# Kernel optimization log

Measured on AMD Instinct MI355X. Metric: run time of the kernel, lower is better.

## Reference

```python
import jax, jax.numpy as jnp
import numpy as np

# ---- model dims (match init_kwargs) ----
N_PER = 10000          # nodes per omic view
NUM_OMICS = 3
N = N_PER * NUM_OMICS  # 30000 total nodes (omic blocks are contiguous)
E = 500000             # edges
R = 6                  # num_relations
HEADS = 1
PROJ = 128             # proj_dim
H0 = 128               # hidden_channels[0]
H1 = 128               # hidden_channels[1]
LABELS = 5
IN_SIZES = [2000, 1500, 1000]
SLOPE = 0.2            # RGATConv leaky_relu negative_slope


def setup_inputs() -> dict:
    key = jax.random.key(0)
    ks = iter(jax.random.split(key, 64))

    def nrm(shape, fan_in):
        return jax.random.normal(next(ks), shape, dtype=jnp.float32) / np.float32(np.sqrt(fan_in))

    inp = {}
    for i, s in enumerate(IN_SIZES):
        inp[f"x{i}"] = jax.random.normal(next(ks), (N_PER, s), dtype=jnp.float32)
    for i, s in enumerate(IN_SIZES):
        inp[f"projW{i}"] = nrm((s, PROJ), s)
        inp[f"projb{i}"] = jnp.zeros((PROJ,), jnp.float32)
    for i in range(NUM_OMICS):
        inp[f"slW{i}"] = nrm((PROJ, H0), PROJ)
        inp[f"slb{i}"] = jnp.zeros((H0,), jnp.float32)
    # RGAT layer 1: weight [R, in, heads*out], q/k [heads*out, heads], bias [heads*out]
    inp["W1"] = nrm((R, PROJ, HEADS * H0), PROJ)
    inp["q1"] = nrm((HEADS * H0, HEADS), H0)
    inp["k1"] = nrm((HEADS * H0, HEADS), H0)
    inp["b1"] = jnp.zeros((HEADS * H0,), jnp.float32)
    # RGAT layer 2: heads=1
    inp["W2"] = nrm((R, HEADS * H0, H1), H0)
    inp["q2"] = nrm((H1, 1), H1)
    inp["k2"] = nrm((H1, 1), H1)
    inp["b2"] = jnp.zeros((H1,), jnp.float32)
    inp["lin1W"] = nrm((H1, H1), H1)
    inp["lin1b"] = jnp.zeros((H1,), jnp.float32)
    inp["lin2W"] = nrm((H1, LABELS), H1)
    inp["lin2b"] = jnp.zeros((LABELS,), jnp.float32)
    inp["edge_src"] = jax.random.randint(next(ks), (E,), 0, N, dtype=jnp.int32)
    inp["edge_dst"] = jax.random.randint(next(ks), (E,), 0, N, dtype=jnp.int32)
    inp["edge_type"] = jax.random.randint(next(ks), (E,), 0, R, dtype=jnp.int32)
    return inp


def _rgat(x, src, dst, etype, W, q, k, b, heads, out_ch):
    """PyG RGATConv: additive-self-attention, across-relation softmax, mod='f-scaled'."""
    # per-relation linear transform of all nodes, then gather per edge
    xw = jnp.einsum('nd,rdo->rno', x, W)          # [R, N, heads*out]
    out_i = xw[etype, dst]                        # [E, heads*out] (target)
    out_j = xw[etype, src]                        # [E, heads*out] (source)
    alpha = jax.nn.leaky_relu(out_i @ q + out_j @ k, SLOPE)   # [E, heads]
    # segment softmax over destination nodes
    m = jax.ops.segment_max(alpha, dst, num_segments=N)
    a = jnp.exp(alpha - m[dst])
    s = jax.ops.segment_sum(a, dst, num_segments=N)
    a = a / s[dst]
    # f-scaled: multiply by in-degree of destination
    deg = jax.ops.segment_sum(jnp.ones((a.shape[0],), a.dtype), dst, num_segments=N)
    a = a * deg[dst][:, None]
    msg = (a[:, :, None] * out_j.reshape(-1, heads, out_ch)).reshape(-1, heads * out_ch)
    return jax.ops.segment_sum(msg, dst, num_segments=N) + b


def reference(x0, x1, x2, projW0, projb0, projW1, projb1, projW2, projb2,
              slW0, slb0, slW1, slb1, slW2, slb2,
              W1, q1, k1, b1, W2, q2, k2, b2,
              lin1W, lin1b, lin2W, lin2b,
              edge_src, edge_dst, edge_type):
    # per-omic projections (ELU)
    xp0 = jax.nn.elu(x0 @ projW0 + projb0)
    xp1 = jax.nn.elu(x1 @ projW1 + projb1)
    xp2 = jax.nn.elu(x2 @ projW2 + projb2)
    x = jnp.concatenate([xp0, xp1, xp2], axis=0)  # [N, PROJ] homogeneous features
    # self-loop contributions (self_loops1 is applied after BOTH convs, on projected x,
    # as in the original forward). Omic node blocks are contiguous.
    sl = jnp.concatenate([xp0 @ slW0 + slb0, xp1 @ slW1 + slb1, xp2 @ slW2 + slb2], axis=0)
    h = jax.nn.elu(_rgat(x, edge_src, edge_dst, edge_type, W1, q1, k1, b1, HEADS, H0) + sl)
    h = jax.nn.elu(_rgat(h, edge_src, edge_dst, edge_type, W2, q2, k2, b2, 1, H1) + sl)
    # classify node_type == 0 nodes (first omic block); dropout p=0.2 is identity at eval
    z = jax.nn.elu(h[:N_PER] @ lin1W + lin1b)
    return z @ lin2W + lin2b
```

## Files before the change

kernel.cpp:

```cpp
#include <hip/hip_runtime.h>
#include <math.h>

#define N_TOTAL 30000
#define NPER 10000
#define NEDGE 500000
#define NREL 6
#define SLOPE 0.2f
#define WCAP 4

typedef __attribute__((ext_vector_type(4))) float f32x4;
typedef __attribute__((ext_vector_type(8))) short s16x8;
typedef __attribute__((ext_vector_type(4))) short s16x4;
typedef unsigned short u16;
typedef unsigned int u32;

__device__ __forceinline__ u16 f2bf(float v) {
  u32 x = __float_as_uint(v);
  u32 r = (x + 0x7fffu + ((x >> 16) & 1u)) >> 16;
  return (u16)r;
}
__device__ __forceinline__ float bf2f(u16 u) {
  return __uint_as_float(((u32)u) << 16);
}

template<bool BIAS, bool ELU, bool ADD, bool SPLITK>
__device__ __forceinline__ void gemm_core(
    const float* __restrict__ A, const u16* __restrict__ Bt,
    const float* __restrict__ bias, const float* __restrict__ add,
    float* __restrict__ C, int M, int K, int Kp, int kbeg, int kend)
{
  __shared__ char As[64 * 128];
  __shared__ char Aslo[64 * 128];
  __shared__ char Bs[128 * 128];
  const int tid = threadIdx.x;
  const int bm = blockIdx.x * 64;
  const int lane = tid & 63;
  const int wave = tid >> 6;
  const int wr = wave >> 1, wc = wave & 1;
  const int lane16 = lane & 15, lhalf = lane >> 4;

  const int a_row0 = tid >> 4;
  const int a_kc = (tid & 15) << 2;
  const int b_row0 = tid >> 3;
  const int b_kc = (tid & 7) << 3;

  float4 pa[4];
  s16x8 pb[4];

  auto LOAD = [&](int k0) {
    #pragma unroll
    for (int it = 0; it < 4; it++) {
      int gr = bm + a_row0 + it * 16, gk = k0 + a_kc;
      float4 v = make_float4(0.f, 0.f, 0.f, 0.f);
      if (gr < M && gk < K) v = *(const float4*)&A[(size_t)gr * K + gk];
      pa[it] = v;
    }
    #pragma unroll
    for (int it = 0; it < 4; it++) {
      int row = b_row0 + it * 32;
      pb[it] = *(const s16x8*)&Bt[(size_t)row * Kp + k0 + b_kc];
    }
  };

  f32x4 acc[2][4];
  #pragma unroll
  for (int mi = 0; mi < 2; mi++)
    #pragma unroll
    for (int ni = 0; ni < 4; ni++)
      #pragma unroll
      for (int q = 0; q < 4; q++) acc[mi][ni][q] = 0.f;

  LOAD(kbeg);

  for (int k0 = kbeg; k0 < kend; k0 += 64) {
    #pragma unroll
    for (int it = 0; it < 4; it++) {
      int row = a_row0 + it * 16;
      float vv[4] = {pa[it].x, pa[it].y, pa[it].z, pa[it].w};
      s16x4 hi, lo;
      #pragma unroll
      for (int j = 0; j < 4; j++) {
        u16 h = f2bf(vv[j]);
        hi[j] = (short)h;
        lo[j] = (short)f2bf(vv[j] - bf2f(h));
      }
      int boff = row * 128 + ((a_kc * 2) ^ ((row & 7) << 4));
      *(s16x4*)(As + boff) = hi;
      *(s16x4*)(Aslo + boff) = lo;
    }
    #pragma unroll
    for (int it = 0; it < 4; it++) {
      int row = b_row0 + it * 32;
      *(s16x8*)(Bs + row * 128 + ((b_kc * 2) ^ ((row & 7) << 4))) = pb[it];
    }
    __syncthreads();
    if (k0 + 64 < kend) LOAD(k0 + 64);
    #pragma unroll
    for (int kk = 0; kk < 2; kk++) {
      const int kbyte = kk * 64 + lhalf * 16;
      s16x8 afh[2], afl[2], bfr[4];
      #pragma unroll
      for (int mi = 0; mi < 2; mi++) {
        int row = wr * 32 + mi * 16 + lane16;
        int boff = row * 128 + (kbyte ^ ((row & 7) << 4));
        afh[mi] = *(const s16x8*)(As + boff);
        afl[mi] = *(const s16x8*)(Aslo + boff);
      }
      #pragma unroll
      for (int ni = 0; ni < 4; ni++) {
        int row = wc * 64 + ni * 16 + lane16;
        bfr[ni] = *(const s16x8*)(Bs + row * 128 + (kbyte ^ ((row & 7) << 4)));
      }
      #pragma unroll
      for (int mi = 0; mi < 2; mi++)
        #pragma unroll
        for (int ni = 0; ni < 4; ni++) {
          acc[mi][ni] = __builtin_amdgcn_mfma_f32_16x16x32_bf16(
              afl[mi], bfr[ni], acc[mi][ni], 0, 0, 0);
          acc[mi][ni] = __builtin_amdgcn_mfma_f32_16x16x32_bf16(
              afh[mi], bfr[ni], acc[mi][ni], 0, 0, 0);
        }
    }
    __syncthreads();
  }

  float bcol[4];
  #pragma unroll
  for (int ni = 0; ni < 4; ni++) {
    int col = wc * 64 + ni * 16 + lane16;
    if (BIAS) bcol[ni] = bias[col];
  }
  #pragma unroll
  for (int mi = 0; mi < 2; mi++) {
    #pragma unroll
    for (int q = 0; q < 4; q++) {
      int grow = bm + wr * 32 + mi * 16 + lhalf * 4 + q;
      if (grow < M) {
        #pragma unroll
        for (int ni = 0; ni < 4; ni++) {
          float v = acc[mi][ni][q];
          int col = wc * 64 + ni * 16 + lane16;
          if (BIAS) v += bcol[ni];
          if (ADD) v += add[(size_t)grow * 128 + col];
          if (!SPLITK && ELU) v = v > 0.f ? v : expm1f(v);
          C[(size_t)grow * 128 + col] = v;
        }
      }
    }
  }
}

struct GB {
  const float* A[3];
  const u16* Bt[3];
  const float* bias[3];
  const float* add[3];
  float* C[3];
  int K[3];
  int Kp[3];
};

template<bool BIAS, bool ELU, bool ADD>
__global__ __launch_bounds__(256, 2)
void gemm_mfma(GB gb, int M)
{
  int z = blockIdx.z;
  gemm_core<BIAS, ELU, ADD, false>(gb.A[z], gb.Bt[z], gb.bias[z], gb.add[z],
                                   gb.C[z], M, gb.K[z], gb.Kp[z], 0, gb.Kp[z]);
}

struct SK {
  const float* A[3];
  const u16* Bt[3];
  float* C[3];
  int K[3];
  int Kp[3];
};

__global__ __launch_bounds__(256, 2)
void gemm_splitk(SK sk, int M)
{
  int z = blockIdx.z;
  int cb = blockIdx.y * 512;
  if (cb >= sk.Kp[z]) return;
  int kend = (cb + 512 < sk.Kp[z]) ? cb + 512 : sk.Kp[z];
  float* C = sk.C[z] + (size_t)blockIdx.y * M * 128;
  gemm_core<false, false, false, true>(sk.A[z], sk.Bt[z], nullptr, nullptr,
                                       C, M, sk.K[z], sk.Kp[z], cb, kend);
}

struct RP { const float* bias[3]; int nch[3]; };

__global__ __launch_bounds__(256)
void reduce_proj(const float* __restrict__ part, RP rp, float* __restrict__ Xf)
{
  int z = blockIdx.z;
  int i = blockIdx.x * 256 + threadIdx.x;
  int c = i & 127;
  int nch = rp.nch[z];
  const float* base = part + (size_t)z * 4 * NPER * 128 + i;
  float s = 0.f;
  for (int ch = 0; ch < nch; ch++) s += base[(size_t)ch * NPER * 128];
  s += rp.bias[z][c];
  Xf[(size_t)z * NPER * 128 + i] = s > 0.f ? s : expm1f(s);
}

struct CW {
  const float* src[9];
  u16* dst[9];
  int K[9];
  int Kp[9];
};

__global__ __launch_bounds__(256)
void conv_w(CW cw) {
  int z = blockIdx.z;
  int K = cw.K[z], Kp = cw.Kp[z];
  int idx = blockIdx.x * 256 + threadIdx.x;
  if (idx >= 128 * Kp) return;
  int kq = idx >> 7, n = idx & 127;
  cw.dst[z][(size_t)n * Kp + kq] =
      (kq < K) ? f2bf(cw.src[z][(size_t)kq * 128 + n]) : (u16)0;
}

__global__ __launch_bounds__(128)
void wqk_kernel(const float* __restrict__ W, const float* __restrict__ q,
                const float* __restrict__ k, float* __restrict__ wq,
                float* __restrict__ wk)
{
  int r = blockIdx.x;
  int t = threadIdx.x;
  const float* Wr = W + (size_t)r * 128 * 128 + (size_t)t * 128;
  float aq = 0.f, ak = 0.f;
  for (int o = 0; o < 128; o++) {
    float w = Wr[o];
    aq = fmaf(w, q[o], aq);
    ak = fmaf(w, k[o], ak);
  }
  wq[r * 128 + t] = aq;
  wk[r * 128 + t] = ak;
}

__global__ __launch_bounds__(256)
void qdkd_kernel(const float* __restrict__ Xf, const float* __restrict__ wq,
                 const float* __restrict__ wk, float* __restrict__ QD,
                 float* __restrict__ KD)
{
  __shared__ float sq[NREL * 128], sk[NREL * 128];
  for (int i = threadIdx.x; i < NREL * 128; i += 256) { sq[i] = wq[i]; sk[i] = wk[i]; }
  __syncthreads();
  int n = blockIdx.x * 256 + threadIdx.x;
  if (n >= N_TOTAL) return;
  float aq[NREL], ak[NREL];
  #pragma unroll
  for (int r = 0; r < NREL; r++) { aq[r] = 0.f; ak[r] = 0.f; }
  for (int kc = 0; kc < 128; kc += 4) {
    float4 x = *(const float4*)&Xf[(size_t)n * 128 + kc];
    #pragma unroll
    for (int r = 0; r < NREL; r++) {
      aq[r] += x.x * sq[r * 128 + kc] + x.y * sq[r * 128 + kc + 1]
             + x.z * sq[r * 128 + kc + 2] + x.w * sq[r * 128 + kc + 3];
      ak[r] += x.x * sk[r * 128 + kc] + x.y * sk[r * 128 + kc + 1]
             + x.z * sk[r * 128 + kc + 2] + x.w * sk[r * 128 + kc + 3];
    }
  }
  #pragma unroll
  for (int r = 0; r < NREL; r++) {
    QD[(size_t)r * N_TOTAL + n] = aq[r];
    KD[(size_t)r * N_TOTAL + n] = ak[r];
  }
}

__global__ __launch_bounds__(256)
void edge_count(const int* __restrict__ dst, int* __restrict__ cnt) {
  int e = blockIdx.x * 256 + threadIdx.x;
  if (e < NEDGE) atomicAdd(&cnt[dst[e]], 1);
}

__global__ __launch_bounds__(1024)
void scan_kernel(const int* __restrict__ cnt, int* __restrict__ off,
                 int* __restrict__ cur) {
  __shared__ int ps[1024];
  const int t = threadIdx.x;
  const int CH = (N_TOTAL + 1023) / 1024;
  const int base = t * CH;
  int s = 0;
  for (int i = 0; i < CH; i++) {
    int idx = base + i;
    if (idx < N_TOTAL) s += cnt[idx];
  }
  ps[t] = s;
  __syncthreads();
  for (int o = 1; o < 1024; o <<= 1) {
    int v = (t >= o) ? ps[t - o] : 0;
    __syncthreads();
    ps[t] += v;
    __syncthreads();
  }
  int run = ps[t] - s;
  for (int i = 0; i < CH; i++) {
    int idx = base + i;
    if (idx < N_TOTAL) {
      off[idx] = run; cur[idx] = run;
      run += cnt[idx];
    }
  }
  if (t == 1023) off[N_TOTAL] = run;
}

__global__ __launch_bounds__(256)
void edge_fill(const int* __restrict__ dst, const int* __restrict__ src,
               const int* __restrict__ et, int* __restrict__ cur,
               int* __restrict__ meta) {
  int e = blockIdx.x * 256 + threadIdx.x;
  if (e >= NEDGE) return;
  int p = atomicAdd(&cur[dst[e]], 1);
  meta[p] = src[e] | (et[e] << 15);
}

__global__ __launch_bounds__(256)
void csr_aggw(const int* __restrict__ off, const int* __restrict__ meta,
              const float* __restrict__ qd, const float* __restrict__ kd,
              const float* __restrict__ xrow, float* __restrict__ agg)
{
  const int d = blockIdx.x * 4 + (threadIdx.x >> 6);
  const int lane = threadIdx.x & 63;
  if (d >= N_TOTAL) return;
  const int n0 = off[d];
  const int deg = off[d + 1] - n0;

  float2 accr[NREL];
  #pragma unroll
  for (int r = 0; r < NREL; r++) accr[r] = make_float2(0.f, 0.f);

  float qrow[NREL];
  #pragma unroll
  for (int r = 0; r < NREL; r++) qrow[r] = qd[r * N_TOTAL + d];

  if (deg > 0) {
    if (deg <= 64 * WCAP) {
      int mreg[WCAP];
      float areg[WCAP];
      const int nc = (deg + 63) >> 6;
      float lmax = -3.0e38f;
      #pragma unroll
      for (int c = 0; c < WCAP; c++) {
        mreg[c] = 0; areg[c] = -3.0e38f;
        int i = c * 64 + lane;
        if (c < nc && i < deg) {
          int mm = meta[n0 + i];
          int s_ = mm & 0x7FFF, t = mm >> 15;
          float a = qrow[t] + kd[t * N_TOTAL + s_];
          a = (a > 0.f) ? a : SLOPE * a;
          mreg[c] = mm; areg[c] = a;
          lmax = fmaxf(lmax, a);
        }
      }
      #pragma unroll
      for (int m = 32; m; m >>= 1) lmax = fmaxf(lmax, __shfl_xor(lmax, m));
      float lsum = 0.f;
      #pragma unroll
      for (int c = 0; c < WCAP; c++) {
        int i = c * 64 + lane;
        if (c < nc && i < deg) {
          areg[c] = expf(areg[c] - lmax);
          lsum += areg[c];
        }
      }
      #pragma unroll
      for (int m = 32; m; m >>= 1) lsum += __shfl_xor(lsum, m);
      const float scale = (float)deg / lsum;
      for (int i = 0; i < deg; i++) {
        int c = i >> 6, l = i & 63;
        float cf = 0.f; int mm = 0;
        #pragma unroll
        for (int cc = 0; cc < WCAP; cc++) {
          if (cc == c) { cf = __shfl(areg[cc], l); mm = __shfl(mreg[cc], l); }
        }
        cf *= scale;
        int s_ = mm & 0x7FFF, t = mm >> 15;
        float2 v = *(const float2*)&xrow[(size_t)s_ * 128 + lane * 2];
        float2 cv = make_float2(cf * v.x, cf * v.y);
        #pragma unroll
        for (int r = 0; r < NREL; r++) {
          bool hit = (t == r);
          accr[r].x += hit ? cv.x : 0.f;
          accr[r].y += hit ? cv.y : 0.f;
        }
      }
    } else {
      float m = -3.0e38f;
      for (int i = 0; i < deg; i++) {
        int mm = meta[n0 + i];
        int s_ = mm & 0x7FFF, t = mm >> 15;
        float a = qrow[t] + kd[t * N_TOTAL + s_];
        a = (a > 0.f) ? a : SLOPE * a;
        m = fmaxf(m, a);
      }
      float ssum = 0.f;
      for (int i = 0; i < deg; i++) {
        int mm = meta[n0 + i];
        int s_ = mm & 0x7FFF, t = mm >> 15;
        float a = qrow[t] + kd[t * N_TOTAL + s_];
        a = (a > 0.f) ? a : SLOPE * a;
        ssum += expf(a - m);
      }
      const float scale = (float)deg / ssum;
      for (int i = 0; i < deg; i++) {
        int mm = meta[n0 + i];
        int s_ = mm & 0x7FFF, t = mm >> 15;
        float a = qrow[t] + kd[t * N_TOTAL + s_];
        a = (a > 0.f) ? a : SLOPE * a;
        float cf = expf(a - m) * scale;
        float2 v = *(const float2*)&xrow[(size_t)s_ * 128 + lane * 2];
        float2 cv = make_float2(cf * v.x, cf * v.y);
        #pragma unroll
        for (int r = 0; r < NREL; r++) {
          bool hit = (t == r);
          accr[r].x += hit ? cv.x : 0.f;
          accr[r].y += hit ? cv.y : 0.f;
        }
      }
    }
  }
  #pragma unroll
  for (int r = 0; r < NREL; r++)
    *(float2*)&agg[((size_t)d * NREL + r) * 128 + lane * 2] = accr[r];
}

__global__ __launch_bounds__(256)
void lin2_kernel(const float* __restrict__ z, const float* __restrict__ W,
                 const float* __restrict__ b, float* __restrict__ out)
{
  int row = blockIdx.x * 4 + (threadIdx.x >> 6);
  int lane = threadIdx.x & 63;
  if (row >= NPER) return;
  float p[5] = {0.f, 0.f, 0.f, 0.f, 0.f};
  #pragma unroll
  for (int h = 0; h < 2; h++) {
    int kidx = lane + h * 64;
    float zv = z[(size_t)row * 128 + kidx];
    #pragma unroll
    for (int j = 0; j < 5; j++) p[j] = fmaf(zv, W[kidx * 5 + j], p[j]);
  }
  #pragma unroll
  for (int mm = 32; mm; mm >>= 1)
    #pragma unroll
    for (int j = 0; j < 5; j++) p[j] += __shfl_xor(p[j], mm);
  if (lane == 0) {
    #pragma unroll
    for (int j = 0; j < 5; j++) out[(size_t)row * 5 + j] = p[j] + b[j];
  }
}

extern "C" void kernel_launch(void* const* d_in, const int* in_sizes, int n_in,
                              void* d_out, int out_size, void* d_ws, size_t ws_size,
                              hipStream_t stream) {
  const float* xs[3] = {(const float*)d_in[0], (const float*)d_in[1], (const float*)d_in[2]};
  const float* projW[3] = {(const float*)d_in[3], (const float*)d_in[5], (const float*)d_in[7]};
  const float* projb[3] = {(const float*)d_in[4], (const float*)d_in[6], (const float*)d_in[8]};
  const float* slW[3]   = {(const float*)d_in[9], (const float*)d_in[11], (const float*)d_in[13]};
  const float* slb[3]   = {(const float*)d_in[10], (const float*)d_in[12], (const float*)d_in[14]};
  const float* W1 = (const float*)d_in[15];
  const float* q1 = (const float*)d_in[16];
  const float* k1 = (const float*)d_in[17];
  const float* b1 = (const float*)d_in[18];
  const float* W2 = (const float*)d_in[19];
  const float* q2 = (const float*)d_in[20];
  const float* k2 = (const float*)d_in[21];
  const float* b2 = (const float*)d_in[22];
  const float* lin1W = (const float*)d_in[23];
  const float* lin1b = (const float*)d_in[24];
  const float* lin2W = (const float*)d_in[25];
  const float* lin2b = (const float*)d_in[26];
  const int* esrc = (const int*)d_in[27];
  const int* edst = (const int*)d_in[28];
  const int* etyp = (const int*)d_in[29];

  char* wp = (char*)d_ws;
  auto alloc = [&](size_t bytes) -> char* {
    char* p = wp; wp += (bytes + 255) & ~(size_t)255; return p;
  };
  float* Xf  = (float*)alloc((size_t)N_TOTAL * 128 * 4);
  float* SL  = (float*)alloc((size_t)N_TOTAL * 128 * 4);
  float* Hf  = (float*)alloc((size_t)N_TOTAL * 128 * 4);
  float* QD  = (float*)alloc((size_t)NREL * N_TOTAL * 4);
  float* KD  = (float*)alloc((size_t)NREL * N_TOTAL * 4);
  float* Z   = (float*)alloc((size_t)NPER * 128 * 4);
  float* WQ1 = (float*)alloc((size_t)NREL * 128 * 4);
  float* WK1 = (float*)alloc((size_t)NREL * 128 * 4);
  float* WQ2 = (float*)alloc((size_t)NREL * 128 * 4);
  float* WK2 = (float*)alloc((size_t)NREL * 128 * 4);
  int*   CNT = (int*)  alloc((size_t)N_TOTAL * 4);
  int*   OFF = (int*)  alloc((size_t)(N_TOTAL + 1) * 4);
  int*   CUR = (int*)  alloc((size_t)N_TOTAL * 4);
  int*   META= (int*)  alloc((size_t)NEDGE * 4);

  float* AGG  = (float*)alloc((size_t)N_TOTAL * NREL * 128 * 4);
  float* PART = AGG;

  CW cw;
  int nW = 0;
  auto addW = [&](const float* src, int K) {
    int Kp = (K + 63) & ~63;
    cw.src[nW] = src; cw.K[nW] = K; cw.Kp[nW] = Kp;
    cw.dst[nW] = (u16*)alloc((size_t)128 * Kp * 2);
    nW++;
  };
  addW(projW[0], 2000); addW(projW[1], 1500); addW(projW[2], 1000);
  addW(slW[0], 128); addW(slW[1], 128); addW(slW[2], 128);
  addW(W1, NREL * 128);
  addW(W2, NREL * 128);
  addW(lin1W, 128);

  const int gridM_per = (NPER + 63) / 64;
  const int gridM_tot = (N_TOTAL + 63) / 64;
  const int gridE = (NEDGE + 255) / 256;

  hipMemsetAsync(CNT, 0, (size_t)N_TOTAL * 4, stream);
  edge_count<<<gridE, 256, 0, stream>>>(edst, CNT);
  scan_kernel<<<1, 1024, 0, stream>>>(CNT, OFF, CUR);
  edge_fill<<<gridE, 256, 0, stream>>>(edst, esrc, etyp, CUR, META);

  conv_w<<<dim3(1024, 1, 9), 256, 0, stream>>>(cw);
  wqk_kernel<<<NREL, 128, 0, stream>>>(W1, q1, k1, WQ1, WK1);
  wqk_kernel<<<NREL, 128, 0, stream>>>(W2, q2, k2, WQ2, WK2);

  {
    SK sk;
    for (int z = 0; z < 3; z++) {
      sk.A[z] = xs[z]; sk.Bt[z] = cw.dst[z];
      sk.C[z] = PART + (size_t)z * 4 * NPER * 128;
      sk.K[z] = cw.K[z]; sk.Kp[z] = cw.Kp[z];
    }
    gemm_splitk<<<dim3(gridM_per, 4, 3), 256, 0, stream>>>(sk, NPER);
    RP rp;
    for (int z = 0; z < 3; z++) { rp.bias[z] = projb[z]; rp.nch[z] = cw.Kp[z] / 512; }
    reduce_proj<<<dim3(NPER * 128 / 256, 1, 3), 256, 0, stream>>>(PART, rp, Xf);
  }
  {
    GB g;
    for (int z = 0; z < 3; z++) {
      g.A[z] = Xf + (size_t)z * NPER * 128; g.Bt[z] = cw.dst[3 + z];
      g.bias[z] = slb[z]; g.add[z] = nullptr;
      g.C[z] = SL + (size_t)z * NPER * 128;
      g.K[z] = 128; g.Kp[z] = 128;
    }
    gemm_mfma<true, false, false><<<dim3(gridM_per, 1, 3), 256, 0, stream>>>(g, NPER);
  }

  for (int layer = 0; layer < 2; layer++) {
    const float* Ain = (layer == 0) ? Xf : Hf;
    const float* WQ = (layer == 0) ? WQ1 : WQ2;
    const float* WK = (layer == 0) ? WK1 : WK2;
    const float* bb = (layer == 0) ? b1 : b2;
    const u16* Wstk = cw.dst[6 + layer];

    qdkd_kernel<<<(N_TOTAL + 255) / 256, 256, 0, stream>>>(Ain, WQ, WK, QD, KD);
    csr_aggw<<<(N_TOTAL + 3) / 4, 256, 0, stream>>>(OFF, META, QD, KD, Ain, AGG);
    GB g;
    g.A[0] = AGG; g.Bt[0] = Wstk; g.bias[0] = bb; g.add[0] = SL; g.C[0] = Hf;
    g.K[0] = NREL * 128; g.Kp[0] = NREL * 128;
    gemm_mfma<true, true, true><<<dim3(gridM_tot, 1, 1), 256, 0, stream>>>(g, N_TOTAL);
  }

  {
    GB g;
    g.A[0] = Hf; g.Bt[0] = cw.dst[8]; g.bias[0] = lin1b; g.add[0] = nullptr; g.C[0] = Z;
    g.K[0] = 128; g.Kp[0] = 128;
    gemm_mfma<true, true, false><<<dim3(gridM_per, 1, 1), 256, 0, stream>>>(g, NPER);
  }
  lin2_kernel<<<(NPER + 3) / 4, 256, 0, stream>>>(Z, lin2W, lin2b, (float*)d_out);
}
```

Before: 432.9 us.

## Double-buffer GEMM register prefetch and split-K the relation transform GEMM

```diff
diff --git a/kernel.cpp b/kernel.cpp
--- a/kernel.cpp
+++ b/kernel.cpp
@@ -23,7 +23,7 @@
   return __uint_as_float(((u32)u) << 16);
 }
 
-template<bool BIAS, bool ELU, bool ADD, bool SPLITK>
+template<bool BIAS, bool ELU, bool ADD, bool RAW>
 __device__ __forceinline__ void gemm_core(
     const float* __restrict__ A, const u16* __restrict__ Bt,
     const float* __restrict__ bias, const float* __restrict__ add,
@@ -44,23 +44,54 @@
   const int b_row0 = tid >> 3;
   const int b_kc = (tid & 7) << 3;
 
-  float4 pa[4];
-  s16x8 pb[4];
-
-  auto LOAD = [&](int k0) {
-    #pragma unroll
-    for (int it = 0; it < 4; it++) {
-      int gr = bm + a_row0 + it * 16, gk = k0 + a_kc;
-      float4 v = make_float4(0.f, 0.f, 0.f, 0.f);
-      if (gr < M && gk < K) v = *(const float4*)&A[(size_t)gr * K + gk];
-      pa[it] = v;
-    }
-    #pragma unroll
-    for (int it = 0; it < 4; it++) {
-      int row = b_row0 + it * 32;
-      pb[it] = *(const s16x8*)&Bt[(size_t)row * Kp + k0 + b_kc];
-    }
+  float4 pa0[4], pa1[4];
+  s16x8 pb0[4], pb1[4];
+
+#define DEF_LOAD(NAME, PA, PB)                                            \
+  auto NAME = [&](int k0) {                                               \
+    _Pragma("unroll")                                                     \
+    for (int it = 0; it < 4; it++) {                                      \
+      int gr = bm + a_row0 + it * 16, gk = k0 + a_kc;                     \
+      float4 v = make_float4(0.f, 0.f, 0.f, 0.f);                         \
+      if (gr < M && gk < K) v = *(const float4*)&A[(size_t)gr * K + gk];  \
+      PA[it] = v;                                                         \
+    }                                                                     \
+    _Pragma("unroll")                                                     \
+    for (int it = 0; it < 4; it++) {                                      \
+      int row = b_row0 + it * 32;                                         \
+      PB[it] = *(const s16x8*)&Bt[(size_t)row * Kp + k0 + b_kc];          \
+    }                                                                     \
   };
+  DEF_LOAD(LOAD0, pa0, pb0)
+  DEF_LOAD(LOAD1, pa1, pb1)
+#undef DEF_LOAD
+
+#define DEF_WRITE(NAME, PA, PB)                                           \
+  auto NAME = [&]() {                                                     \
+    _Pragma("unroll")                                                     \
+    for (int it = 0; it < 4; it++) {                                      \
+      int row = a_row0 + it * 16;                                         \
+      float vv[4] = {PA[it].x, PA[it].y, PA[it].z, PA[it].w};             \
+      s16x4 hi, lo;                                                       \
+      _Pragma("unroll")                                                   \
+      for (int j = 0; j < 4; j++) {                                       \
+        u16 h = f2bf(vv[j]);                                              \
+        hi[j] = (short)h;                                                 \
+        lo[j] = (short)f2bf(vv[j] - bf2f(h));                             \
+      }                                                                   \
+      int boff = row * 128 + ((a_kc * 2) ^ ((row & 7) << 4));             \
+      *(s16x4*)(As + boff) = hi;                                          \
+      *(s16x4*)(Aslo + boff) = lo;                                        \
+    }                                                                     \
+    _Pragma("unroll")                                                     \
+    for (int it = 0; it < 4; it++) {                                      \
+      int row = b_row0 + it * 32;                                         \
+      *(s16x8*)(Bs + row * 128 + ((b_kc * 2) ^ ((row & 7) << 4))) = PB[it]; \
+    }                                                                     \
+  };
+  DEF_WRITE(WRITE0, pa0, pb0)
+  DEF_WRITE(WRITE1, pa1, pb1)
+#undef DEF_WRITE
 
   f32x4 acc[2][4];
   #pragma unroll
@@ -70,31 +101,7 @@
       #pragma unroll
       for (int q = 0; q < 4; q++) acc[mi][ni][q] = 0.f;
 
-  LOAD(kbeg);
-
-  for (int k0 = kbeg; k0 < kend; k0 += 64) {
-    #pragma unroll
-    for (int it = 0; it < 4; it++) {
-      int row = a_row0 + it * 16;
-      float vv[4] = {pa[it].x, pa[it].y, pa[it].z, pa[it].w};
-      s16x4 hi, lo;
-      #pragma unroll
-      for (int j = 0; j < 4; j++) {
-        u16 h = f2bf(vv[j]);
-        hi[j] = (short)h;
-        lo[j] = (short)f2bf(vv[j] - bf2f(h));
-      }
-      int boff = row * 128 + ((a_kc * 2) ^ ((row & 7) << 4));
-      *(s16x4*)(As + boff) = hi;
-      *(s16x4*)(Aslo + boff) = lo;
-    }
-    #pragma unroll
-    for (int it = 0; it < 4; it++) {
-      int row = b_row0 + it * 32;
-      *(s16x8*)(Bs + row * 128 + ((b_kc * 2) ^ ((row & 7) << 4))) = pb[it];
-    }
-    __syncthreads();
-    if (k0 + 64 < kend) LOAD(k0 + 64);
+  auto MFMA = [&]() {
     #pragma unroll
     for (int kk = 0; kk < 2; kk++) {
       const int kbyte = kk * 64 + lhalf * 16;
@@ -121,7 +128,25 @@
               afh[mi], bfr[ni], acc[mi][ni], 0, 0, 0);
         }
     }
+  };
+
+  const int nt = (kend - kbeg) >> 6;
+  LOAD0(kbeg);
+  if (nt > 1) LOAD1(kbeg + 64);
+
+  for (int t = 0; t < nt; t += 2) {
+    if (t) __syncthreads();
+    WRITE0();
     __syncthreads();
+    if (t + 2 < nt) LOAD0(kbeg + (t + 2) * 64);
+    MFMA();
+    if (t + 1 < nt) {
+      __syncthreads();
+      WRITE1();
+      __syncthreads();
+      if (t + 3 < nt) LOAD1(kbeg + (t + 3) * 64);
+      MFMA();
+    }
   }
 
   float bcol[4];
@@ -142,7 +167,7 @@
           int col = wc * 64 + ni * 16 + lane16;
           if (BIAS) v += bcol[ni];
           if (ADD) v += add[(size_t)grow * 128 + col];
-          if (!SPLITK && ELU) v = v > 0.f ? v : expm1f(v);
+          if (!RAW && ELU) v = v > 0.f ? v : expm1f(v);
           C[(size_t)grow * 128 + col] = v;
         }
       }
@@ -178,12 +203,12 @@
 };
 
 __global__ __launch_bounds__(256, 2)
-void gemm_splitk(SK sk, int M)
+void gemm_splitk(SK sk, int M, int chunk)
 {
   int z = blockIdx.z;
-  int cb = blockIdx.y * 512;
+  int cb = blockIdx.y * chunk;
   if (cb >= sk.Kp[z]) return;
-  int kend = (cb + 512 < sk.Kp[z]) ? cb + 512 : sk.Kp[z];
+  int kend = (cb + chunk < sk.Kp[z]) ? cb + chunk : sk.Kp[z];
   float* C = sk.C[z] + (size_t)blockIdx.y * M * 128;
   gemm_core<false, false, false, true>(sk.A[z], sk.Bt[z], nullptr, nullptr,
                                        C, M, sk.K[z], sk.Kp[z], cb, kend);
@@ -203,6 +228,15 @@
   for (int ch = 0; ch < nch; ch++) s += base[(size_t)ch * NPER * 128];
   s += rp.bias[z][c];
   Xf[(size_t)z * NPER * 128 + i] = s > 0.f ? s : expm1f(s);
+}
+
+__global__ __launch_bounds__(256)
+void reduce_tr(const float* __restrict__ part, const float* __restrict__ bias,
+               const float* __restrict__ sl, float* __restrict__ h)
+{
+  int i = blockIdx.x * 256 + threadIdx.x;
+  float v = part[i] + part[(size_t)N_TOTAL * 128 + i] + bias[i & 127] + sl[i];
+  h[i] = v > 0.f ? v : expm1f(v);
 }
 
 struct CW {
@@ -496,8 +530,8 @@
   int*   CUR = (int*)  alloc((size_t)N_TOTAL * 4);
   int*   META= (int*)  alloc((size_t)NEDGE * 4);
 
+  float* PART = (float*)alloc((size_t)3 * 4 * NPER * 128 * 4);
   float* AGG  = (float*)alloc((size_t)N_TOTAL * NREL * 128 * 4);
-  float* PART = AGG;
 
   CW cw;
   int nW = 0;
@@ -533,7 +567,7 @@
       sk.C[z] = PART + (size_t)z * 4 * NPER * 128;
       sk.K[z] = cw.K[z]; sk.Kp[z] = cw.Kp[z];
     }
-    gemm_splitk<<<dim3(gridM_per, 4, 3), 256, 0, stream>>>(sk, NPER);
+    gemm_splitk<<<dim3(gridM_per, 4, 3), 256, 0, stream>>>(sk, NPER, 512);
     RP rp;
     for (int z = 0; z < 3; z++) { rp.bias[z] = projb[z]; rp.nch[z] = cw.Kp[z] / 512; }
     reduce_proj<<<dim3(NPER * 128 / 256, 1, 3), 256, 0, stream>>>(PART, rp, Xf);
@@ -558,10 +592,11 @@
 
     qdkd_kernel<<<(N_TOTAL + 255) / 256, 256, 0, stream>>>(Ain, WQ, WK, QD, KD);
     csr_aggw<<<(N_TOTAL + 3) / 4, 256, 0, stream>>>(OFF, META, QD, KD, Ain, AGG);
-    GB g;
-    g.A[0] = AGG; g.Bt[0] = Wstk; g.bias[0] = bb; g.add[0] = SL; g.C[0] = Hf;
-    g.K[0] = NREL * 128; g.Kp[0] = NREL * 128;
-    gemm_mfma<true, true, true><<<dim3(gridM_tot, 1, 1), 256, 0, stream>>>(g, N_TOTAL);
+    SK sk;
+    sk.A[0] = AGG; sk.Bt[0] = Wstk; sk.C[0] = PART;
+    sk.K[0] = NREL * 128; sk.Kp[0] = NREL * 128;
+    gemm_splitk<<<dim3(gridM_tot, 2, 1), 256, 0, stream>>>(sk, N_TOTAL, 384);
+    reduce_tr<<<(N_TOTAL * 128) / 256, 256, 0, stream>>>(PART, bb, SL, Hf);
   }
 
   {
```

Measured after the change: 459.0 us. 6.0% more time.
